# Optimization experiments

Hardware: AMD Instinct MI355X
Metric: run time of the kernel (lower is better)

Reference implementation:

```python
import jax, jax.numpy as jnp
import numpy as np

B, N = 512, 4
OBS, OBSU, ID = 128, 64, 16
STATE = OBS + OBSU - ID  # 176
M1, M2, G1, A = 256, 256, 256, 16
E = 128  # hypernet_embed


def setup_inputs() -> dict:
    key = jax.random.key(0)
    ks = jax.random.split(key, 24)

    def W(k, shape):
        return jax.random.normal(k, shape, dtype=jnp.float32) * 0.05

    inp = {"input": jax.random.normal(ks[0], (B, N, OBS + OBSU), dtype=jnp.float32)}
    # layer1_hypernet: Linear(ID, 10*E)
    inp["l1_W"] = W(ks[1], (10 * E, ID)); inp["l1_b"] = W(ks[2], (10 * E,))
    # hyper_net{i}_w / hyper_net{i}_b : Linear(E, in*out) / Linear(E, out)
    inp["w1W"] = W(ks[3], (STATE * M1, E)); inp["w1b"] = W(ks[4], (STATE * M1,))
    inp["b1W"] = W(ks[5], (M1, E));        inp["b1b"] = W(ks[6], (M1,))
    inp["w2W"] = W(ks[7], (M1 * M2, E));   inp["w2b"] = W(ks[8], (M1 * M2,))
    inp["b2W"] = W(ks[9], (M2, E));        inp["b2b"] = W(ks[10], (M2,))
    inp["w3W"] = W(ks[11], (M2 * M2, E));  inp["w3b"] = W(ks[12], (M2 * M2,))
    inp["b3W"] = W(ks[13], (M2, E));       inp["b3b"] = W(ks[14], (M2,))
    inp["w4W"] = W(ks[15], (M2 * G1, E));  inp["w4b"] = W(ks[16], (M2 * G1,))
    inp["b4W"] = W(ks[17], (G1, E));       inp["b4b"] = W(ks[18], (G1,))
    inp["w5W"] = W(ks[19], (G1 * A, E));   inp["w5b"] = W(ks[20], (G1 * A,))
    inp["b5W"] = W(ks[21], (A, E));        inp["b5b"] = W(ks[22], (A,))
    return inp


def reference(input, l1_W, l1_b, w1W, w1b, b1W, b1b, w2W, w2b, b2W, b2b,
              w3W, w3b, b3W, b3b, w4W, w4b, b4W, b4b, w5W, w5b, b5W, b5b):
    b, n, d = input.shape
    BN = b * n
    ids = input[..., -ID:].reshape(BN, ID)
    x = input[..., :-ID].reshape(BN, d - ID)  # [BN, STATE]
    # layer1_hypernet: ReLU(Linear(ID -> 10E))
    h = jax.nn.relu(ids @ l1_W.T + l1_b)  # [BN, 10E]
    chunk = lambda i: h[:, i * E:(i + 1) * E]

    def layer(x, iw, ib, wW, wb, bW, bb, out_dim, act):
        # generate per-sample weight [BN, in, out] and bias [BN, out]
        Wm = (chunk(iw) @ wW.T + wb).reshape(BN, x.shape[-1], out_dim)
        bm = chunk(ib) @ bW.T + bb
        y = jnp.einsum('bs,bsm->bm', x, Wm) + bm  # batched GEMV
        return jax.nn.relu(y) if act else y

    out = layer(x,   0, 1, w1W, w1b, b1W, b1b, M1, True)
    out = layer(out, 2, 3, w2W, w2b, b2W, b2b, M2, True)
    out = layer(out, 4, 5, w3W, w3b, b3W, b3b, M2, True)
    out = layer(out, 6, 7, w4W, w4b, b4W, b4b, G1, False)  # no ReLU after layer 4
    out = layer(out, 8, 9, w5W, w5b, b5W, b5b, A, True)
    return out.reshape(b, n, A)
```

## Files before the change

### kernel.cpp

```cpp
#include <hip/hip_runtime.h>
#include <hip/hip_bf16.h>

#define E_ 128
#define NSAMP 2048

typedef __attribute__((ext_vector_type(8))) short short8;
typedef __attribute__((ext_vector_type(4))) float floatx4;

__device__ __forceinline__ ushort f2b(float f) {
    union { __hip_bfloat16 h; ushort u; } cv;
    cv.h = __float2bfloat16(f);
    return cv.u;
}

__device__ __forceinline__ void gload_lds16(const ushort* g, ushort* l) {
    __builtin_amdgcn_global_load_lds(
        (const __attribute__((address_space(1))) void*)g,
        (__attribute__((address_space(3))) void*)l, 16, 0, 0);
}

__global__ void hyper_h(const float* __restrict__ input, const float* __restrict__ l1W,
                        const float* __restrict__ l1b, float* __restrict__ h)
{
    int b = blockIdx.x / 5;
    int o = (blockIdx.x % 5) * 256 + threadIdx.x;
    const float* ids = input + (size_t)b * 192 + 176;
    const float* w = l1W + (size_t)o * 16;
    float a = l1b[o];
#pragma unroll
    for (int i = 0; i < 16; i += 4) {
        float4 wv = *(const float4*)(w + i);
        a += ids[i] * wv.x + ids[i + 1] * wv.y + ids[i + 2] * wv.z + ids[i + 3] * wv.w;
    }
    h[(size_t)b * 1280 + o] = fmaxf(a, 0.f);
}

__global__ void x0_t(const float* __restrict__ input, float* __restrict__ xT0)
{
    int idx = blockIdx.x * 256 + threadIdx.x;
    int s = idx >> 11, b = idx & 2047;
    xT0[idx] = input[(size_t)b * 192 + s];
}

__global__ void cvt_bf16(const float* __restrict__ src, ushort* __restrict__ dst, int n)
{
    int i = (blockIdx.x * 256 + threadIdx.x) * 8;
    if (i >= n) return;
    float4 a = *(const float4*)(src + i);
    float4 b = *(const float4*)(src + i + 4);
    union { ushort o[8]; uint4 v; } u;
    u.o[0] = f2b(a.x); u.o[1] = f2b(a.y); u.o[2] = f2b(a.z); u.o[3] = f2b(a.w);
    u.o[4] = f2b(b.x); u.o[5] = f2b(b.y); u.o[6] = f2b(b.z); u.o[7] = f2b(b.w);
    *(uint4*)(dst + i) = u.v;
}

__global__ void cvt_bias(const float* __restrict__ bW, const float* __restrict__ wb,
                         ushort* __restrict__ dst, int S, int M)
{
    int idx = blockIdx.x * 256 + threadIdx.x;
    int slice = idx / (M * E_);
    int rem = idx - slice * (M * E_);
    int m = rem / E_, e = rem - m * E_;
    ushort v;
    if (slice == 0) {
        v = f2b(bW[(size_t)m * E_ + e]);
    } else {
        int s = (slice - 1) * 128 + e;
        v = (s < S) ? f2b(wb[(size_t)s * M + m]) : (ushort)0;
    }
    dst[(size_t)(S + slice) * M * E_ + rem] = v;
}

__global__ __launch_bounds__(256, 2) void gemm_big(
    const ushort* __restrict__ wWb, const float* __restrict__ h,
    const float* __restrict__ xT, float* __restrict__ partial,
    int S, int iw, int ksplit, int btiles, int ntiles)
{
    __shared__ __align__(16) ushort Bs[4 * 128 * 64];
    __shared__ __align__(16) float xs[17 * 128];

    const int tid = threadIdx.x;
    const int bid = blockIdx.x;
    const int xcd = bid & 7;
    const int jj_ = bid >> 3;
    const int combo = xcd + 8 * (jj_ / btiles);
    const int bt = jj_ % btiles;
    const int nt = combo % ntiles;
    const int ks = combo / ntiles;
    const int b0 = bt * 128;
    const int m0 = nt * 128;
    const int total_s = S + 3;
    const int base = total_s / ksplit;
    const int rem = total_s - base * ksplit;
    const int s0 = ks * base + min(ks, rem);
    const int s1v = s0 + base + (ks < rem ? 1 : 0);
    const int sE = min(s1v, S);
    const int ns = sE - s0;
    const int T = 2 * ns;

    const int lane = tid & 63;
    const int wave = tid >> 6;
    const int quad = lane >> 4;
    const int lr = lane & 15;
    const int wm0 = wave * 32;

    const int brow = lane >> 3;
    const int bgg = (lane & 7) ^ brow;

    float hreg[2][2][2][8];
#pragma unroll
    for (int i = 0; i < 2; ++i)
#pragma unroll
        for (int p = 0; p < 2; ++p)
#pragma unroll
            for (int kk = 0; kk < 2; ++kk) {
                const float* src = h + (size_t)(b0 + wm0 + i * 16 + lr) * 1280
                                     + (size_t)iw * E_ + p * 64 + kk * 32 + quad * 8;
                float4 v0 = *(const float4*)(src);
                float4 v1 = *(const float4*)(src + 4);
                hreg[i][p][kk][0] = v0.x; hreg[i][p][kk][1] = v0.y;
                hreg[i][p][kk][2] = v0.z; hreg[i][p][kk][3] = v0.w;
                hreg[i][p][kk][4] = v1.x; hreg[i][p][kk][5] = v1.y;
                hreg[i][p][kk][6] = v1.z; hreg[i][p][kk][7] = v1.w;
            }

    for (int idx = tid; idx < ns * 128; idx += 256) {
        int j = idx >> 7, bb2 = idx & 127;
        xs[idx] = xT[(size_t)(s0 + j) * NSAMP + b0 + bb2];
    }

    floatx4 acc[2][8];
#pragma unroll
    for (int i = 0; i < 2; ++i)
#pragma unroll
        for (int j = 0; j < 8; ++j)
            acc[i][j] = (floatx4){0.f, 0.f, 0.f, 0.f};

    auto dmaB = [&](int s, int p, ushort* buf) {
#pragma unroll
        for (int t4 = 0; t4 < 4; ++t4) {
            int rloc = wave * 32 + t4 * 8;
            const ushort* gp = wWb + ((size_t)s * 256 + m0 + rloc + brow) * E_ + p * 64 + bgg * 8;
            gload_lds16(gp, buf + (size_t)rloc * 64 + lane * 8);
        }
    };

    __builtin_amdgcn_sched_barrier(0);
    __syncthreads();
    __builtin_amdgcn_sched_barrier(0);
#pragma unroll
    for (int pt = 0; pt < 3; ++pt)
        if (pt < T) dmaB(s0 + (pt >> 1), pt & 1, Bs + (size_t)(pt & 3) * (128 * 64));

    for (int si = 0; si < ns; ++si) {
        float xr0 = 0.f, xr1 = 0.f;
#pragma unroll
        for (int P = 0; P < 2; ++P) {
            const int t2 = 2 * si + P;
            const int left = T - 1 - t2;
            if (left >= 2)      asm volatile("s_waitcnt vmcnt(8)" ::: "memory");
            else if (left == 1) asm volatile("s_waitcnt vmcnt(4)" ::: "memory");
            else                asm volatile("s_waitcnt vmcnt(0)" ::: "memory");
            __builtin_amdgcn_sched_barrier(0);
            __builtin_amdgcn_s_barrier();
            __builtin_amdgcn_sched_barrier(0);

            if (t2 + 3 < T) {
                const int tn = t2 + 3;
                dmaB(s0 + (tn >> 1), tn & 1, Bs + (size_t)(tn & 3) * (128 * 64));
            }
            if (P == 0) {
                xr0 = xs[si * 128 + wm0 + lr];
                xr1 = xs[si * 128 + wm0 + 16 + lr];
            }
            const ushort* bcur = Bs + (size_t)(t2 & 3) * (128 * 64);
#pragma unroll
            for (int kk = 0; kk < 2; ++kk) {
                short8 bfr[8];
#pragma unroll
                for (int j = 0; j < 8; ++j) {
                    const int row = j * 16 + lr;
                    const int swz = ((kk * 4 + quad) ^ (lr & 7)) * 8;
                    bfr[j] = *(const short8*)&bcur[(size_t)row * 64 + swz];
                }
                short8 af0, af1;
#pragma unroll
                for (int jj = 0; jj < 8; ++jj) {
                    af0[jj] = (short)f2b(xr0 * hreg[0][P][kk][jj]);
                    af1[jj] = (short)f2b(xr1 * hreg[1][P][kk][jj]);
                }
#pragma unroll
                for (int j = 0; j < 8; ++j) {
                    acc[0][j] = __builtin_amdgcn_mfma_f32_16x16x32_bf16(af0, bfr[j], acc[0][j], 0, 0, 0);
                    acc[1][j] = __builtin_amdgcn_mfma_f32_16x16x32_bf16(af1, bfr[j], acc[1][j], 0, 0, 0);
                }
            }
        }
    }

    for (int s = sE; s < s1v; ++s) {
        for (int p = 0; p < 2; ++p) {
            __syncthreads();
            dmaB(s, p, Bs);
            short8 af[2][2];
            if (s == S) {
#pragma unroll
                for (int kk = 0; kk < 2; ++kk)
#pragma unroll
                    for (int i = 0; i < 2; ++i) {
                        const float* src = h + (size_t)(b0 + wm0 + i * 16 + lr) * 1280
                                             + (size_t)(iw + 1) * E_ + p * 64 + kk * 32 + quad * 8;
                        float4 v0 = *(const float4*)(src);
                        float4 v1 = *(const float4*)(src + 4);
                        af[kk][i][0] = (short)f2b(v0.x); af[kk][i][1] = (short)f2b(v0.y);
                        af[kk][i][2] = (short)f2b(v0.z); af[kk][i][3] = (short)f2b(v0.w);
                        af[kk][i][4] = (short)f2b(v1.x); af[kk][i][5] = (short)f2b(v1.y);
                        af[kk][i][6] = (short)f2b(v1.z); af[kk][i][7] = (short)f2b(v1.w);
                    }
            } else {
                const int jbase = (s - S - 1) * 128 + p * 64;
#pragma unroll
                for (int kk = 0; kk < 2; ++kk)
#pragma unroll
                    for (int i = 0; i < 2; ++i) {
                        const int b = b0 + wm0 + i * 16 + lr;
#pragma unroll
                        for (int jj = 0; jj < 8; ++jj) {
                            const int sp = jbase + kk * 32 + quad * 8 + jj;
                            af[kk][i][jj] = (sp < S) ? (short)f2b(xT[(size_t)sp * NSAMP + b]) : (short)0;
                        }
                    }
            }
            __syncthreads();
#pragma unroll
            for (int kk = 0; kk < 2; ++kk) {
                short8 bfr[8];
#pragma unroll
                for (int j = 0; j < 8; ++j) {
                    const int row = j * 16 + lr;
                    const int swz = ((kk * 4 + quad) ^ (lr & 7)) * 8;
                    bfr[j] = *(const short8*)&Bs[(size_t)row * 64 + swz];
                }
#pragma unroll
                for (int j = 0; j < 8; ++j) {
                    acc[0][j] = __builtin_amdgcn_mfma_f32_16x16x32_bf16(af[kk][0], bfr[j], acc[0][j], 0, 0, 0);
                    acc[1][j] = __builtin_amdgcn_mfma_f32_16x16x32_bf16(af[kk][1], bfr[j], acc[1][j], 0, 0, 0);
                }
            }
        }
    }

    float* dst = partial + (size_t)ks * NSAMP * 256;
#pragma unroll
    for (int i = 0; i < 2; ++i)
#pragma unroll
        for (int j = 0; j < 8; ++j)
#pragma unroll
            for (int r = 0; r < 4; ++r) {
                const int row = wm0 + i * 16 + quad * 4 + r;
                const int col = j * 16 + lr;
                dst[(size_t)(b0 + row) * 256 + m0 + col] = acc[i][j][r];
            }
}

template<int BM, int BN, int WROWS, int WCOLS>
__global__ __launch_bounds__(256, 2) void gemm_k(
    const ushort* __restrict__ wWb, const float* __restrict__ h,
    const float* __restrict__ xT, float* __restrict__ partial,
    int S, int M, int iw, int ksplit, int btiles, int ntiles)
{
    constexpr int SM = BM / WROWS / 16;
    constexpr int SN = BN / WCOLS / 16;
    constexpr int ASLOTS = BM * 8 / 256;
    constexpr int LDA = 72;

    __shared__ ushort As[BM][LDA];
    __shared__ ushort Bs[BN][LDA];

    const int tid = threadIdx.x;
    const int bt = blockIdx.x % btiles;
    const int nt = (blockIdx.x / btiles) % ntiles;
    const int ks = blockIdx.x / (btiles * ntiles);
    const int b0 = bt * BM;
    const int m0 = nt * BN;
    const int total_s = S + 3;
    const int base = total_s / ksplit;
    const int rem = total_s - base * ksplit;
    const int s0 = ks * base + min(ks, rem);
    const int s1 = s0 + base + (ks < rem ? 1 : 0);

    const int lane = tid & 63;
    const int wave = tid >> 6;
    const int quad = lane >> 4;
    const int lr = lane & 15;
    const int wm0 = (wave / WCOLS) * (BM / WROWS);
    const int wn0 = (wave % WCOLS) * (BN / WCOLS);

    const int tb = tid >> 3;
    const int teg = tid & 7;

    float hreg[ASLOTS][2][8];
#pragma unroll
    for (int k2 = 0; k2 < ASLOTS; ++k2) {
        int b = tb + 32 * k2;
#pragma unroll
        for (int p = 0; p < 2; ++p) {
            const float* src = h + (size_t)(b0 + b) * 1280 + (size_t)iw * E_ + p * 64 + teg * 8;
            float4 v0 = *(const float4*)(src);
            float4 v1 = *(const float4*)(src + 4);
            hreg[k2][p][0] = v0.x; hreg[k2][p][1] = v0.y; hreg[k2][p][2] = v0.z; hreg[k2][p][3] = v0.w;
            hreg[k2][p][4] = v1.x; hreg[k2][p][5] = v1.y; hreg[k2][p][6] = v1.z; hreg[k2][p][7] = v1.w;
        }
    }

    floatx4 acc[SM][SN];
#pragma unroll
    for (int i = 0; i < SM; ++i)
#pragma unroll
        for (int j = 0; j < SN; ++j)
            acc[i][j] = (floatx4){0.f, 0.f, 0.f, 0.f};

    for (int s = s0; s < s1; ++s) {
        float xv[ASLOTS];
        if (s < S) {
#pragma unroll
            for (int k2 = 0; k2 < ASLOTS; ++k2)
                xv[k2] = xT[(size_t)s * NSAMP + b0 + tb + 32 * k2];
        }

#pragma unroll
        for (int p = 0; p < 2; ++p) {
            if (s < S) {
#pragma unroll
                for (int k2 = 0; k2 < ASLOTS; ++k2) {
                    union { ushort o[8]; uint4 v; } u;
#pragma unroll
                    for (int j = 0; j < 8; ++j) u.o[j] = f2b(xv[k2] * hreg[k2][p][j]);
                    *(uint4*)&As[tb + 32 * k2][teg * 8] = u.v;
                }
            } else if (s == S) {
#pragma unroll
                for (int k2 = 0; k2 < ASLOTS; ++k2) {
                    const float* src = h + (size_t)(b0 + tb + 32 * k2) * 1280
                                         + (size_t)(iw + 1) * E_ + p * 64 + teg * 8;
                    float4 v0 = *(const float4*)(src);
                    float4 v1 = *(const float4*)(src + 4);
                    union { ushort o[8]; uint4 v; } u;
                    u.o[0] = f2b(v0.x); u.o[1] = f2b(v0.y); u.o[2] = f2b(v0.z); u.o[3] = f2b(v0.w);
                    u.o[4] = f2b(v1.x); u.o[5] = f2b(v1.y); u.o[6] = f2b(v1.z); u.o[7] = f2b(v1.w);
                    *(uint4*)&As[tb + 32 * k2][teg * 8] = u.v;
                }
            } else {
                int j0 = (s - S - 1) * 128 + p * 64 + teg * 8;
#pragma unroll
                for (int k2 = 0; k2 < ASLOTS; ++k2) {
                    int b = b0 + tb + 32 * k2;
                    union { ushort o[8]; uint4 v; } u;
#pragma unroll
                    for (int jj = 0; jj < 8; ++jj) {
                        int sp = j0 + jj;
                        u.o[jj] = (sp < S) ? f2b(xT[(size_t)sp * NSAMP + b]) : (ushort)0;
                    }
                    *(uint4*)&As[tb + 32 * k2][teg * 8] = u.v;
                }
            }
#pragma unroll
            for (int slot = tid; slot < BN * 8; slot += 256) {
                int m = slot >> 3, eg2 = slot & 7;
                *(uint4*)&Bs[m][eg2 * 8] =
                    *(const uint4*)(wWb + ((size_t)s * M + m0 + m) * E_ + p * 64 + eg2 * 8);
            }
            __syncthreads();
#pragma unroll
            for (int kk = 0; kk < 2; ++kk) {
                short8 af[SM], bfr[SN];
#pragma unroll
                for (int i = 0; i < SM; ++i)
                    af[i] = *(const short8*)&As[wm0 + i * 16 + lr][kk * 32 + quad * 8];
#pragma unroll
                for (int j = 0; j < SN; ++j)
                    bfr[j] = *(const short8*)&Bs[wn0 + j * 16 + lr][kk * 32 + quad * 8];
#pragma unroll
                for (int i = 0; i < SM; ++i)
#pragma unroll
                    for (int j = 0; j < SN; ++j)
                        acc[i][j] = __builtin_amdgcn_mfma_f32_16x16x32_bf16(af[i], bfr[j], acc[i][j], 0, 0, 0);
            }
            __syncthreads();
        }
    }

    float* dst = partial + (size_t)ks * NSAMP * M;
#pragma unroll
    for (int i = 0; i < SM; ++i)
#pragma unroll
        for (int j = 0; j < SN; ++j)
#pragma unroll
            for (int r = 0; r < 4; ++r) {
                int row = wm0 + i * 16 + quad * 4 + r;
                int col = wn0 + j * 16 + lr;
                dst[(size_t)(b0 + row) * M + m0 + col] = acc[i][j][r];
            }
}

__global__ void reduce_mid(const float* __restrict__ partial, const float* __restrict__ bb,
                           float* __restrict__ xTn, int KS, int relu)
{
    __shared__ float t[32][33];
    const int b0 = (blockIdx.x >> 3) * 32;
    const int m0 = (blockIdx.x & 7) * 32;
    const int mo = threadIdx.x & 31;
    const int bs0 = threadIdx.x >> 5;
    const float bv = bb[m0 + mo];
#pragma unroll
    for (int r = 0; r < 4; ++r) {
        const int bs = bs0 + 8 * r;
        const size_t off = (size_t)(b0 + bs) * 256 + m0 + mo;
        float a0 = 0.f, a1 = 0.f, a2 = 0.f, a3 = 0.f;
#pragma unroll
        for (int k = 0; k < 16; k += 4) {
            a0 += partial[(size_t)(k + 0) * (NSAMP * 256) + off];
            a1 += partial[(size_t)(k + 1) * (NSAMP * 256) + off];
            a2 += partial[(size_t)(k + 2) * (NSAMP * 256) + off];
            a3 += partial[(size_t)(k + 3) * (NSAMP * 256) + off];
        }
        float a = (a0 + a1) + (a2 + a3) + bv;
        if (relu) a = fmaxf(a, 0.f);
        t[bs][mo] = a;
    }
    __syncthreads();
    const int bo = threadIdx.x & 31;
    const int ms0 = threadIdx.x >> 5;
#pragma unroll
    for (int r = 0; r < 4; ++r) {
        const int ms = ms0 + 8 * r;
        xTn[(size_t)(m0 + ms) * NSAMP + b0 + bo] = t[bo][ms];
    }
}

__global__ void reduce_out(const float* __restrict__ partial, const float* __restrict__ bb,
                           float* __restrict__ out, int KS)
{
    int idx = blockIdx.x * 256 + threadIdx.x;
    float a0 = 0.f, a1 = 0.f, a2 = 0.f, a3 = 0.f;
#pragma unroll
    for (int k = 0; k < 64; k += 4) {
        a0 += partial[(size_t)(k + 0) * (NSAMP * 16) + idx];
        a1 += partial[(size_t)(k + 1) * (NSAMP * 16) + idx];
        a2 += partial[(size_t)(k + 2) * (NSAMP * 16) + idx];
        a3 += partial[(size_t)(k + 3) * (NSAMP * 16) + idx];
    }
    out[idx] = fmaxf((a0 + a1) + (a2 + a3) + bb[idx & 15], 0.f);
}

extern "C" void kernel_launch(void* const* d_in, const int* in_sizes, int n_in,
                              void* d_out, int out_size, void* d_ws, size_t ws_size,
                              hipStream_t stream)
{
    const float* input = (const float*)d_in[0];
    const float* l1W   = (const float*)d_in[1];
    const float* l1b   = (const float*)d_in[2];

    char* ws = (char*)d_ws;
    ushort* wWb = (ushort*)(ws + 0);
    float* h    = (float*)(ws + 16975872);
    float* xT0  = (float*)(ws + 27461632);
    float* xT1  = (float*)(ws + 29558784);
    float* part = (float*)(ws + 31655936);

    hipLaunchKernelGGL(hyper_h, dim3(2048 * 5), dim3(256), 0, stream, input, l1W, l1b, h);
    hipLaunchKernelGGL(x0_t, dim3(176 * 2048 / 256), dim3(256), 0, stream, input, xT0);

    const int S_[5] = {176, 256, 256, 256, 256};
    const int M_[5] = {256, 256, 256, 256, 16};
    float* xt[2] = {xT0, xT1};

    for (int i = 0; i < 5; ++i) {
        const float* wW = (const float*)d_in[3 + 4 * i];
        const float* wb = (const float*)d_in[4 + 4 * i];
        const float* bW = (const float*)d_in[5 + 4 * i];
        const float* bb = (const float*)d_in[6 + 4 * i];
        float* xin = xt[i & 1];
        int n = S_[i] * M_[i] * E_;
        hipLaunchKernelGGL(cvt_bf16, dim3(n / 2048), dim3(256), 0, stream, wW, wWb, n);
        hipLaunchKernelGGL(cvt_bias, dim3(3 * M_[i] * E_ / 256), dim3(256), 0, stream,
                           bW, wb, wWb, S_[i], M_[i]);

        if (M_[i] == 256) {
            const int btiles = 16, ntiles = 2, ksplit = 16;
            hipLaunchKernelGGL(gemm_big, dim3(btiles * ntiles * ksplit), dim3(256), 0, stream,
                               wWb, h, xin, part, S_[i], 2 * i, ksplit, btiles, ntiles);
            hipLaunchKernelGGL(reduce_mid, dim3(512), dim3(256), 0, stream,
                               part, bb, xt[(i + 1) & 1], ksplit, (i < 3) ? 1 : 0);
        } else {
            const int btiles = 8, ntiles = 1, ksplit = 64;
            hipLaunchKernelGGL((gemm_k<256, 16, 4, 1>), dim3(btiles * ntiles * ksplit), dim3(256), 0, stream,
                               wWb, h, xin, part, S_[i], 16, 2 * i, ksplit, btiles, ntiles);
            hipLaunchKernelGGL(reduce_out, dim3(128), dim3(256), 0, stream,
                               part, bb, (float*)d_out, ksplit);
        }
    }
}
```

Before: 527.5 us.

## Fuse weight/bias conversion kernels and restructure gemm_big to per-state double buffering

```diff
diff --git a/kernel.cpp b/kernel.cpp
--- a/kernel.cpp
+++ b/kernel.cpp
@@ -42,33 +42,38 @@
     xT0[idx] = input[(size_t)b * 192 + s];
 }
 
-__global__ void cvt_bf16(const float* __restrict__ src, ushort* __restrict__ dst, int n)
+__global__ void cvt_layer(const float* __restrict__ wW, const float* __restrict__ wb,
+                          const float* __restrict__ bW, ushort* __restrict__ dst,
+                          int S, int M)
 {
     int i = (blockIdx.x * 256 + threadIdx.x) * 8;
-    if (i >= n) return;
-    float4 a = *(const float4*)(src + i);
-    float4 b = *(const float4*)(src + i + 4);
+    const int nW = S * M * E_;
     union { ushort o[8]; uint4 v; } u;
-    u.o[0] = f2b(a.x); u.o[1] = f2b(a.y); u.o[2] = f2b(a.z); u.o[3] = f2b(a.w);
-    u.o[4] = f2b(b.x); u.o[5] = f2b(b.y); u.o[6] = f2b(b.z); u.o[7] = f2b(b.w);
+    if (i < nW) {
+        float4 a = *(const float4*)(wW + i);
+        float4 b = *(const float4*)(wW + i + 4);
+        u.o[0] = f2b(a.x); u.o[1] = f2b(a.y); u.o[2] = f2b(a.z); u.o[3] = f2b(a.w);
+        u.o[4] = f2b(b.x); u.o[5] = f2b(b.y); u.o[6] = f2b(b.z); u.o[7] = f2b(b.w);
+    } else {
+        int rem = i - nW;
+        int slice = rem / (M * E_);
+        int r2 = rem - slice * (M * E_);
+        int m = r2 >> 7, e = r2 & 127;
+        if (slice == 0) {
+            const float* src = bW + (size_t)m * E_ + e;
+            float4 a = *(const float4*)(src);
+            float4 b = *(const float4*)(src + 4);
+            u.o[0] = f2b(a.x); u.o[1] = f2b(a.y); u.o[2] = f2b(a.z); u.o[3] = f2b(a.w);
+            u.o[4] = f2b(b.x); u.o[5] = f2b(b.y); u.o[6] = f2b(b.z); u.o[7] = f2b(b.w);
+        } else {
+#pragma unroll
+            for (int jj = 0; jj < 8; ++jj) {
+                int s = (slice - 1) * 128 + e + jj;
+                u.o[jj] = (s < S) ? f2b(wb[(size_t)s * M + m]) : (ushort)0;
+            }
+        }
+    }
     *(uint4*)(dst + i) = u.v;
-}
-
-__global__ void cvt_bias(const float* __restrict__ bW, const float* __restrict__ wb,
-                         ushort* __restrict__ dst, int S, int M)
-{
-    int idx = blockIdx.x * 256 + threadIdx.x;
-    int slice = idx / (M * E_);
-    int rem = idx - slice * (M * E_);
-    int m = rem / E_, e = rem - m * E_;
-    ushort v;
-    if (slice == 0) {
-        v = f2b(bW[(size_t)m * E_ + e]);
-    } else {
-        int s = (slice - 1) * 128 + e;
-        v = (s < S) ? f2b(wb[(size_t)s * M + m]) : (ushort)0;
-    }
-    dst[(size_t)(S + slice) * M * E_ + rem] = v;
 }
 
 __global__ __launch_bounds__(256, 2) void gemm_big(
@@ -76,7 +81,7 @@
     const float* __restrict__ xT, float* __restrict__ partial,
     int S, int iw, int ksplit, int btiles, int ntiles)
 {
-    __shared__ __align__(16) ushort Bs[4 * 128 * 64];
+    __shared__ __align__(16) ushort Bs[2][2 * 128 * 64];
     __shared__ __align__(16) float xs[17 * 128];
 
     const int tid = threadIdx.x;
@@ -96,7 +101,6 @@
     const int s1v = s0 + base + (ks < rem ? 1 : 0);
     const int sE = min(s1v, S);
     const int ns = sE - s0;
-    const int T = 2 * ns;
 
     const int lane = tid & 63;
     const int wave = tid >> 6;
@@ -113,15 +117,15 @@
 #pragma unroll
         for (int p = 0; p < 2; ++p)
 #pragma unroll
-            for (int kk = 0; kk < 2; ++kk) {
+            for (int k2 = 0; k2 < 2; ++k2) {
                 const float* src = h + (size_t)(b0 + wm0 + i * 16 + lr) * 1280
-                                     + (size_t)iw * E_ + p * 64 + kk * 32 + quad * 8;
+                                     + (size_t)iw * E_ + p * 64 + k2 * 32 + quad * 8;
                 float4 v0 = *(const float4*)(src);
                 float4 v1 = *(const float4*)(src + 4);
-                hreg[i][p][kk][0] = v0.x; hreg[i][p][kk][1] = v0.y;
-                hreg[i][p][kk][2] = v0.z; hreg[i][p][kk][3] = v0.w;
-                hreg[i][p][kk][4] = v1.x; hreg[i][p][kk][5] = v1.y;
-                hreg[i][p][kk][6] = v1.z; hreg[i][p][kk][7] = v1.w;
+                hreg[i][p][k2][0] = v0.x; hreg[i][p][k2][1] = v0.y;
+                hreg[i][p][k2][2] = v0.z; hreg[i][p][k2][3] = v0.w;
+                hreg[i][p][k2][4] = v1.x; hreg[i][p][k2][5] = v1.y;
+                hreg[i][p][k2][6] = v1.z; hreg[i][p][k2][7] = v1.w;
             }
 
     for (int idx = tid; idx < ns * 128; idx += 256) {
@@ -136,7 +140,17 @@
         for (int j = 0; j < 8; ++j)
             acc[i][j] = (floatx4){0.f, 0.f, 0.f, 0.f};
 
-    auto dmaB = [&](int s, int p, ushort* buf) {
+    auto dmaB = [&](int s, ushort* buf) {
+#pragma unroll
+        for (int p = 0; p < 2; ++p)
+#pragma unroll
+            for (int t4 = 0; t4 < 4; ++t4) {
+                int rloc = wave * 32 + t4 * 8;
+                const ushort* gp = wWb + ((size_t)s * 256 + m0 + rloc + brow) * E_ + p * 64 + bgg * 8;
+                gload_lds16(gp, buf + (size_t)p * 8192 + (size_t)rloc * 64 + lane * 8);
+            }
+    };
+    auto dmaBh = [&](int s, int p, ushort* buf) {
 #pragma unroll
         for (int t4 = 0; t4 < 4; ++t4) {
             int rloc = wave * 32 + t4 * 8;
@@ -148,103 +162,102 @@
     __builtin_amdgcn_sched_barrier(0);
     __syncthreads();
     __builtin_amdgcn_sched_barrier(0);
-#pragma unroll
-    for (int pt = 0; pt < 3; ++pt)
-        if (pt < T) dmaB(s0 + (pt >> 1), pt & 1, Bs + (size_t)(pt & 3) * (128 * 64));
+    dmaB(s0, &Bs[0][0]);
+    if (ns > 1) dmaB(s0 + 1, &Bs[1][0]);
 
     for (int si = 0; si < ns; ++si) {
-        float xr0 = 0.f, xr1 = 0.f;
-#pragma unroll
-        for (int P = 0; P < 2; ++P) {
-            const int t2 = 2 * si + P;
-            const int left = T - 1 - t2;
-            if (left >= 2)      asm volatile("s_waitcnt vmcnt(8)" ::: "memory");
-            else if (left == 1) asm volatile("s_waitcnt vmcnt(4)" ::: "memory");
-            else                asm volatile("s_waitcnt vmcnt(0)" ::: "memory");
-            __builtin_amdgcn_sched_barrier(0);
-            __builtin_amdgcn_s_barrier();
-            __builtin_amdgcn_sched_barrier(0);
-
-            if (t2 + 3 < T) {
-                const int tn = t2 + 3;
-                dmaB(s0 + (tn >> 1), tn & 1, Bs + (size_t)(tn & 3) * (128 * 64));
-            }
-            if (P == 0) {
-                xr0 = xs[si * 128 + wm0 + lr];
-                xr1 = xs[si * 128 + wm0 + 16 + lr];
-            }
-            const ushort* bcur = Bs + (size_t)(t2 & 3) * (128 * 64);
-#pragma unroll
-            for (int kk = 0; kk < 2; ++kk) {
-                short8 bfr[8];
+        const float xr0 = xs[si * 128 + wm0 + lr];
+        const float xr1 = xs[si * 128 + wm0 + 16 + lr];
+        short8 af0[2][2], af1[2][2];
+#pragma unroll
+        for (int p = 0; p < 2; ++p)
+#pragma unroll
+            for (int k2 = 0; k2 < 2; ++k2)
 #pragma unroll
                 for (int j = 0; j < 8; ++j) {
-                    const int row = j * 16 + lr;
-                    const int swz = ((kk * 4 + quad) ^ (lr & 7)) * 8;
-                    bfr[j] = *(const short8*)&bcur[(size_t)row * 64 + swz];
+                    af0[p][k2][j] = (short)f2b(xr0 * hreg[0][p][k2][j]);
+                    af1[p][k2][j] = (short)f2b(xr1 * hreg[1][p][k2][j]);
                 }
-                short8 af0, af1;
-#pragma unroll
-                for (int jj = 0; jj < 8; ++jj) {
-                    af0[jj] = (short)f2b(xr0 * hreg[0][P][kk][jj]);
-                    af1[jj] = (short)f2b(xr1 * hreg[1][P][kk][jj]);
-                }
-#pragma unroll
-                for (int j = 0; j < 8; ++j) {
-                    acc[0][j] = __builtin_amdgcn_mfma_f32_16x16x32_bf16(af0, bfr[j], acc[0][j], 0, 0, 0);
-                    acc[1][j] = __builtin_amdgcn_mfma_f32_16x16x32_bf16(af1, bfr[j], acc[1][j], 0, 0, 0);
-                }
-            }
-        }
+
+        if (si + 1 < ns) asm volatile("s_waitcnt vmcnt(8)" ::: "memory");
+        else             asm volatile("s_waitcnt vmcnt(0)" ::: "memory");
+        __builtin_amdgcn_sched_barrier(0);
+        __builtin_amdgcn_s_barrier();
+        __builtin_amdgcn_sched_barrier(0);
+
+        const ushort* bcur = &Bs[si & 1][0];
+        __builtin_amdgcn_s_setprio(1);
+#pragma unroll
+        for (int kk = 0; kk < 4; ++kk) {
+            const int p = kk >> 1, k2 = kk & 1;
+            const int swz = ((k2 * 4 + quad) ^ (lr & 7)) * 8;
+            short8 bfr[8];
+#pragma unroll
+            for (int j = 0; j < 8; ++j)
+                bfr[j] = *(const short8*)&bcur[(size_t)p * 8192 + (size_t)(j * 16 + lr) * 64 + swz];
+            const short8 a0 = (p == 0) ? ((k2 == 0) ? af0[0][0] : af0[0][1])
+                                       : ((k2 == 0) ? af0[1][0] : af0[1][1]);
+            const short8 a1 = (p == 0) ? ((k2 == 0) ? af1[0][0] : af1[0][1])
+                                       : ((k2 == 0) ? af1[1][0] : af1[1][1]);
+#pragma unroll
+            for (int j = 0; j < 8; ++j) {
+                acc[0][j] = __builtin_amdgcn_mfma_f32_16x16x32_bf16(a0, bfr[j], acc[0][j], 0, 0, 0);
+                acc[1][j] = __builtin_amdgcn_mfma_f32_16x16x32_bf16(a1, bfr[j], acc[1][j], 0, 0, 0);
+            }
+        }
+        __builtin_amdgcn_s_setprio(0);
+        __builtin_amdgcn_sched_barrier(0);
+        __builtin_amdgcn_s_barrier();
+        __builtin_amdgcn_sched_barrier(0);
+
+        if (si + 2 < ns) dmaB(s0 + si + 2, &Bs[si & 1][0]);
     }
 
     for (int s = sE; s < s1v; ++s) {
         for (int p = 0; p < 2; ++p) {
             __syncthreads();
-            dmaB(s, p, Bs);
+            dmaBh(s, p, &Bs[0][0]);
             short8 af[2][2];
             if (s == S) {
 #pragma unroll
-                for (int kk = 0; kk < 2; ++kk)
+                for (int k2 = 0; k2 < 2; ++k2)
 #pragma unroll
                     for (int i = 0; i < 2; ++i) {
                         const float* src = h + (size_t)(b0 + wm0 + i * 16 + lr) * 1280
-                                             + (size_t)(iw + 1) * E_ + p * 64 + kk * 32 + quad * 8;
+                                             + (size_t)(iw + 1) * E_ + p * 64 + k2 * 32 + quad * 8;
                         float4 v0 = *(const float4*)(src);
                         float4 v1 = *(const float4*)(src + 4);
-                        af[kk][i][0] = (short)f2b(v0.x); af[kk][i][1] = (short)f2b(v0.y);
-                        af[kk][i][2] = (short)f2b(v0.z); af[kk][i][3] = (short)f2b(v0.w);
-                        af[kk][i][4] = (short)f2b(v1.x); af[kk][i][5] = (short)f2b(v1.y);
-                        af[kk][i][6] = (short)f2b(v1.z); af[kk][i][7] = (short)f2b(v1.w);
+                        af[k2][i][0] = (short)f2b(v0.x); af[k2][i][1] = (short)f2b(v0.y);
+                        af[k2][i][2] = (short)f2b(v0.z); af[k2][i][3] = (short)f2b(v0.w);
+                        af[k2][i][4] = (short)f2b(v1.x); af[k2][i][5] = (short)f2b(v1.y);
+                        af[k2][i][6] = (short)f2b(v1.z); af[k2][i][7] = (short)f2b(v1.w);
                     }
             } else {
                 const int jbase = (s - S - 1) * 128 + p * 64;
 #pragma unroll
-                for (int kk = 0; kk < 2; ++kk)
+                for (int k2 = 0; k2 < 2; ++k2)
 #pragma unroll
                     for (int i = 0; i < 2; ++i) {
                         const int b = b0 + wm0 + i * 16 + lr;
 #pragma unroll
                         for (int jj = 0; jj < 8; ++jj) {
-                            const int sp = jbase + kk * 32 + quad * 8 + jj;
-                            af[kk][i][jj] = (sp < S) ? (short)f2b(xT[(size_t)sp * NSAMP + b]) : (short)0;
+                            const int sp = jbase + k2 * 32 + quad * 8 + jj;
+                            af[k2][i][jj] = (sp < S) ? (short)f2b(xT[(size_t)sp * NSAMP + b]) : (short)0;
                         }
                     }
             }
             __syncthreads();
 #pragma unroll
-            for (int kk = 0; kk < 2; ++kk) {
+            for (int k2 = 0; k2 < 2; ++k2) {
+                const int swz = ((k2 * 4 + quad) ^ (lr & 7)) * 8;
                 short8 bfr[8];
 #pragma unroll
+                for (int j = 0; j < 8; ++j)
+                    bfr[j] = *(const short8*)&Bs[0][(size_t)(j * 16 + lr) * 64 + swz];
+#pragma unroll
                 for (int j = 0; j < 8; ++j) {
-                    const int row = j * 16 + lr;
-                    const int swz = ((kk * 4 + quad) ^ (lr & 7)) * 8;
-                    bfr[j] = *(const short8*)&Bs[(size_t)row * 64 + swz];
-                }
-#pragma unroll
-                for (int j = 0; j < 8; ++j) {
-                    acc[0][j] = __builtin_amdgcn_mfma_f32_16x16x32_bf16(af[kk][0], bfr[j], acc[0][j], 0, 0, 0);
-                    acc[1][j] = __builtin_amdgcn_mfma_f32_16x16x32_bf16(af[kk][1], bfr[j], acc[1][j], 0, 0, 0);
+                    acc[0][j] = __builtin_amdgcn_mfma_f32_16x16x32_bf16(af[k2][0], bfr[j], acc[0][j], 0, 0, 0);
+                    acc[1][j] = __builtin_amdgcn_mfma_f32_16x16x32_bf16(af[k2][1], bfr[j], acc[1][j], 0, 0, 0);
                 }
             }
         }
@@ -481,10 +494,9 @@
         const float* bW = (const float*)d_in[5 + 4 * i];
         const float* bb = (const float*)d_in[6 + 4 * i];
         float* xin = xt[i & 1];
-        int n = S_[i] * M_[i] * E_;
-        hipLaunchKernelGGL(cvt_bf16, dim3(n / 2048), dim3(256), 0, stream, wW, wWb, n);
-        hipLaunchKernelGGL(cvt_bias, dim3(3 * M_[i] * E_ / 256), dim3(256), 0, stream,
-                           bW, wb, wWb, S_[i], M_[i]);
+        int ntot = (S_[i] + 3) * M_[i] * E_;
+        hipLaunchKernelGGL(cvt_layer, dim3(ntot / 2048), dim3(256), 0, stream,
+                           wW, wb, bW, wWb, S_[i], M_[i]);
 
         if (M_[i] == 256) {
             const int btiles = 16, ntiles = 2, ksplit = 16;
```

Measured after the change: 533.1 us. About the same (+1.1%).
